# Kernel optimization log

Hardware: AMD Instinct MI355X
Metric: run time of the kernel (lower is better)

Reference implementation:

```python
import jax, jax.numpy as jnp
import numpy as np
import math

EPS = 1.1920929e-07  # torch.finfo(float32).eps, used by nn.RMSNorm when eps=None
N_HEADS = 16

def _rmsnorm(x, w):
    return x * jax.lax.rsqrt(jnp.mean(x * x, axis=-1, keepdims=True) + EPS) * w

def setup_inputs() -> dict:
    key = jax.random.key(0)
    D, V, FF = 1024, 32000, 2048
    NS, IPS = 4, 8
    B, T = 2, 1024
    ks = jax.random.split(key, 8)
    sd = 0.02
    g = lambda i, shape: jax.random.normal(ks[i], shape, jnp.float32) * sd
    return {
        "tokens": jax.random.randint(ks[0], (B, T), 0, V),
        "embed_w": g(1, (V, D)),
        "qkv_w": g(2, (3 * D, D)),
        "o_w": g(3, (D, D)),
        "gate_w": g(4, (FF, D)),
        "up_w": g(5, (FF, D)),
        "down_w": g(6, (D, FF)),
        "norm1_w": jnp.ones((D,), jnp.float32),
        "norm2_w": jnp.ones((D,), jnp.float32),
        "scale_gamma": jnp.ones((NS, D), jnp.float32),
        "scale_beta": jnp.zeros((NS, D), jnp.float32),
        "iter_scale": jnp.ones((NS, IPS), jnp.float32),
        "norm_w": jnp.ones((D,), jnp.float32),
        "lm_head_w": g(7, (V, D)),
    }

def _block(x, gamma, beta, qkv_w, o_w, gate_w, up_w, down_w, norm1_w, norm2_w):
    B, T, D = x.shape
    hd = D // N_HEADS
    # pre-attn norm + FiLM modulation
    h = _rmsnorm(x, norm1_w) * gamma + beta
    qkv = (h @ qkv_w.T).reshape(B, T, 3, N_HEADS, hd)
    q = jnp.transpose(qkv[:, :, 0], (0, 2, 1, 3))  # [B,H,T,hd]
    k = jnp.transpose(qkv[:, :, 1], (0, 2, 1, 3))
    v = jnp.transpose(qkv[:, :, 2], (0, 2, 1, 3))
    scores = jnp.einsum('bhqd,bhkd->bhqk', q, k) / math.sqrt(hd)
    causal = jnp.tril(jnp.ones((T, T), dtype=bool))
    scores = jnp.where(causal, scores, -jnp.inf)
    attn = jax.nn.softmax(scores, axis=-1)
    out = jnp.einsum('bhqk,bhkd->bhqd', attn, v)
    out = jnp.transpose(out, (0, 2, 1, 3)).reshape(B, T, D)
    x = x + out @ o_w.T
    # pre-FFN norm + FiLM modulation, SwiGLU
    h2 = _rmsnorm(x, norm2_w) * gamma + beta
    x = x + (jax.nn.silu(h2 @ gate_w.T) * (h2 @ up_w.T)) @ down_w.T
    return x

def reference(tokens, embed_w, qkv_w, o_w, gate_w, up_w, down_w, norm1_w,
              norm2_w, scale_gamma, scale_beta, iter_scale, norm_w, lm_head_w):
    NS, IPS = iter_scale.shape
    x = embed_w[tokens].astype(jnp.float32)  # [B,T,D]
    # flatten (scale, iter) schedule to per-virtual-layer params [NS*IPS, ...]
    gammas = jnp.repeat(scale_gamma, IPS, axis=0)
    betas = jnp.repeat(scale_beta, IPS, axis=0)
    iters = iter_scale.reshape(-1)

    @jax.checkpoint
    def step(x, per):
        g, b, s = per
        y = _block(x, g, b, qkv_w, o_w, gate_w, up_w, down_w, norm1_w, norm2_w)
        return x + (y - x) * s, None

    x, _ = jax.lax.scan(step, x, (gammas, betas, iters))
    return _rmsnorm(x, norm_w) @ lm_head_w.T  # [B,T,V]
```

## Files before the change

kernel.cpp:

```cpp
#include <hip/hip_runtime.h>

typedef __bf16 bf16;
typedef __attribute__((ext_vector_type(8))) __bf16 bf16x8;
typedef __attribute__((ext_vector_type(4))) __bf16 bf16x4;
typedef __attribute__((ext_vector_type(4))) float f32x4;

#define MFMA16(a,b,c) __builtin_amdgcn_mfma_f32_16x16x32_bf16((a),(b),(c),0,0,0)

__device__ __forceinline__ void gload16(const void* g, void* l) {
    __builtin_amdgcn_global_load_lds((const __attribute__((address_space(1))) void*)g,
                                     (__attribute__((address_space(3))) void*)l, 16, 0, 0);
}

__device__ __forceinline__ int xcd_swizzle(int orig, int nwg) {
    int q = nwg >> 3, r = nwg & 7;
    int xcd = orig & 7, loc = orig >> 3;
    int base = (xcd < r) ? xcd * (q + 1) : r * (q + 1) + (xcd - r) * q;
    return base + loc;
}


__global__ __launch_bounds__(256) void cvt_kernel(const float* __restrict__ in,
                                                  bf16* __restrict__ out, int n4) {
    int stride = gridDim.x * 256;
    for (int i = blockIdx.x * 256 + threadIdx.x; i < n4; i += stride) {
        float4 v = ((const float4*)in)[i];
        bf16x4 o;
        o[0] = (bf16)v.x; o[1] = (bf16)v.y; o[2] = (bf16)v.z; o[3] = (bf16)v.w;
        ((bf16x4*)out)[i] = o;
    }
}

__global__ __launch_bounds__(256) void embed_kernel(const int* __restrict__ tok,
                                                    const float* __restrict__ ew,
                                                    float* __restrict__ X) {
    int m = blockIdx.x;
    int t = tok[m];
    ((float4*)(X + (size_t)m * 1024))[threadIdx.x] =
        ((const float4*)(ew + (size_t)t * 1024))[threadIdx.x];
}

template <bool FILM>
__global__ __launch_bounds__(256) void rmsnorm_kernel(const float* __restrict__ X,
                                                      const float* __restrict__ w,
                                                      const float* __restrict__ gamma,
                                                      const float* __restrict__ beta,
                                                      bf16* __restrict__ H) {
    int m = blockIdx.x, t = threadIdx.x;
    float4 xv = ((const float4*)(X + (size_t)m * 1024))[t];
    float ss = xv.x * xv.x + xv.y * xv.y + xv.z * xv.z + xv.w * xv.w;
#pragma unroll
    for (int off = 1; off < 64; off <<= 1) ss += __shfl_xor(ss, off);
    __shared__ float red[4];
    if ((t & 63) == 0) red[t >> 6] = ss;
    __syncthreads();
    float tot = red[0] + red[1] + red[2] + red[3];
    float sc = rsqrtf(tot * (1.0f / 1024.0f) + 1.1920929e-07f);
    float4 wv = ((const float4*)w)[t];
    float r0 = xv.x * sc * wv.x, r1 = xv.y * sc * wv.y;
    float r2 = xv.z * sc * wv.z, r3 = xv.w * sc * wv.w;
    if (FILM) {
        float4 gv = ((const float4*)gamma)[t];
        float4 bv = ((const float4*)beta)[t];
        r0 = r0 * gv.x + bv.x; r1 = r1 * gv.y + bv.y;
        r2 = r2 * gv.z + bv.z; r3 = r3 * gv.w + bv.w;
    }
    bf16x4 o;
    o[0] = (bf16)r0; o[1] = (bf16)r1; o[2] = (bf16)r2; o[3] = (bf16)r3;
    ((bf16x4*)(H + (size_t)m * 1024))[t] = o;
}


__global__ __launch_bounds__(256) void vtrans_kernel(const bf16* __restrict__ QKV,
                                                     bf16* __restrict__ VT) {
    const int tt = blockIdx.x, bh = blockIdx.y;
    const int b = bh >> 4, h = bh & 15;
    __shared__ __align__(16) bf16 Ls[64 * 72];
    const int tid = threadIdx.x;
#pragma unroll
    for (int i = 0; i < 2; ++i) {
        int cid = tid + 256 * i;
        int r = cid >> 3, c8 = (cid & 7) * 8;
        *(bf16x8*)(Ls + r * 72 + c8) =
            *(const bf16x8*)(QKV + (size_t)(b * 1024 + tt * 64 + r) * 3072 + 2048 + h * 64 + c8);
    }
    __syncthreads();
#pragma unroll
    for (int i = 0; i < 2; ++i) {
        int cid = tid + 256 * i;
        int d = cid >> 3, k8 = (cid & 7) * 8;
        bf16x8 v;
#pragma unroll
        for (int j = 0; j < 8; ++j) v[j] = Ls[(k8 + j) * 72 + d];
        *(bf16x8*)(VT + (size_t)bh * 65536 + (size_t)d * 1024 + tt * 64 + k8) = v;
    }
}


template <int MT, int MODE, bool BNF>
__global__ __launch_bounds__(256, 2) void gemm_bt(const bf16* __restrict__ A,
                                                  const bf16* __restrict__ B,
                                                  int GN, int GM,
                                                  int N, int K,
                                                  bf16* __restrict__ Cb, float* __restrict__ Cf,
                                                  const float* __restrict__ Xin,
                                                  const float* __restrict__ Xin2,
                                                  float* __restrict__ Xout,
                                                  const float* __restrict__ sptr) {
    constexpr int BM = 32 * MT;
    __shared__ __align__(16) bf16 As[2][BM * 64];
    __shared__ __align__(16) bf16 Bs[2][128 * 64];
    const int wg = xcd_swizzle(blockIdx.x, GN * GM);
    int bn, bm;
    if (BNF) { bm = wg / GN; bn = wg - bm * GN; }
    else     { bn = wg / GM; bm = wg - bn * GM; }
    const int tid = threadIdx.x, lane = tid & 63, w = tid >> 6;
    const int wr = w >> 1, wc = w & 1, lr = lane & 15, lg = lane >> 4;
    const bf16* Ab = A + (size_t)bm * BM * K;
    const bf16* Bb = B + (size_t)bn * 128 * K;

    f32x4 acc[MT][4];
#pragma unroll
    for (int i = 0; i < MT; ++i)
#pragma unroll
        for (int j = 0; j < 4; ++j) acc[i][j] = (f32x4){0.f, 0.f, 0.f, 0.f};

#define STAGE_AB(buf, ktv)                                                        \
    do {                                                                          \
        _Pragma("unroll")                                                         \
        for (int i = 0; i < MT; ++i) {                                            \
            int cw = i * 256 + w * 64; int cid = cw + lane;                       \
            gload16(Ab + (size_t)(cid >> 3) * K + (ktv) + (cid & 7) * 8,          \
                    As[buf] + cw * 8);                                            \
        }                                                                         \
        _Pragma("unroll")                                                         \
        for (int i = 0; i < 4; ++i) {                                             \
            int cw = i * 256 + w * 64; int cid = cw + lane;                       \
            gload16(Bb + (size_t)(cid >> 3) * K + (ktv) + (cid & 7) * 8,          \
                    Bs[buf] + cw * 8);                                            \
        }                                                                         \
    } while (0)

    STAGE_AB(0, 0);
    __syncthreads();
    int cur = 0;
    for (int kt = 0; kt < K; kt += 64) {
        if (kt + 64 < K) STAGE_AB(cur ^ 1, kt + 64);
        const bf16* Asc = As[cur];
        const bf16* Bsc = Bs[cur];
#pragma unroll
        for (int kk = 0; kk < 64; kk += 32) {
            bf16x8 af[MT], bfr[4];
#pragma unroll
            for (int mi = 0; mi < MT; ++mi)
                af[mi] = *(const bf16x8*)(Asc + (wr * (16 * MT) + mi * 16 + lr) * 64 + kk + lg * 8);
#pragma unroll
            for (int ni = 0; ni < 4; ++ni)
                bfr[ni] = *(const bf16x8*)(Bsc + (wc * 64 + ni * 16 + lr) * 64 + kk + lg * 8);
#pragma unroll
            for (int mi = 0; mi < MT; ++mi)
#pragma unroll
                for (int ni = 0; ni < 4; ++ni)
                    acc[mi][ni] = MFMA16(af[mi], bfr[ni], acc[mi][ni]);
        }
        __syncthreads();
        cur ^= 1;
    }
#undef STAGE_AB

    float s1 = (MODE == 2) ? sptr[0] : 0.f;
#pragma unroll
    for (int mi = 0; mi < MT; ++mi) {
#pragma unroll
        for (int ni = 0; ni < 4; ++ni) {
#pragma unroll
            for (int j = 0; j < 4; ++j) {
                int row = bm * BM + wr * (16 * MT) + mi * 16 + lg * 4 + j;
                int col = bn * 128 + wc * 64 + ni * 16 + lr;
                size_t idx = (size_t)row * N + col;
                float v = acc[mi][ni][j];
                if (MODE == 0) Cb[idx] = (bf16)v;
                else if (MODE == 1) Xout[idx] = Xin[idx] + v;
                else if (MODE == 2) Xout[idx] = Xin[idx] + s1 * (Xin2[idx] - Xin[idx] + v);
                else Cf[idx] = v;
            }
        }
    }
}


__global__ __launch_bounds__(256, 2) void gemm_gateup(const bf16* __restrict__ A,
                                                      const bf16* __restrict__ Bg,
                                                      const bf16* __restrict__ Bu,
                                                      bf16* __restrict__ FF) {
    const int K = 1024, N = 2048;
    __shared__ __align__(16) bf16 As[2][64 * 64];
    __shared__ __align__(16) bf16 Gs[2][128 * 64];
    __shared__ __align__(16) bf16 Us[2][128 * 64];
    const int wg = xcd_swizzle(blockIdx.x, 512);
    const int bn = wg >> 5, bm = wg & 31;
    const int tid = threadIdx.x, lane = tid & 63, w = tid >> 6;
    const int wr = w >> 1, wc = w & 1, lr = lane & 15, lg = lane >> 4;
    const bf16* Ab = A + (size_t)bm * 64 * K;
    const bf16* Gb = Bg + (size_t)bn * 128 * K;
    const bf16* Ub = Bu + (size_t)bn * 128 * K;

    f32x4 ag[2][4], au[2][4];
#pragma unroll
    for (int i = 0; i < 2; ++i)
#pragma unroll
        for (int j = 0; j < 4; ++j) {
            ag[i][j] = (f32x4){0.f, 0.f, 0.f, 0.f};
            au[i][j] = (f32x4){0.f, 0.f, 0.f, 0.f};
        }

#define STAGE_GU(buf, ktv)                                                        \
    do {                                                                          \
        _Pragma("unroll")                                                         \
        for (int i = 0; i < 2; ++i) {                                             \
            int cw = i * 256 + w * 64; int cid = cw + lane;                       \
            gload16(Ab + (size_t)(cid >> 3) * K + (ktv) + (cid & 7) * 8,          \
                    As[buf] + cw * 8);                                            \
        }                                                                         \
        _Pragma("unroll")                                                         \
        for (int i = 0; i < 4; ++i) {                                             \
            int cw = i * 256 + w * 64; int cid = cw + lane;                       \
            size_t ro = (size_t)(cid >> 3) * K + (ktv) + (cid & 7) * 8;           \
            gload16(Gb + ro, Gs[buf] + cw * 8);                                   \
            gload16(Ub + ro, Us[buf] + cw * 8);                                   \
        }                                                                         \
    } while (0)

    STAGE_GU(0, 0);
    __syncthreads();
    int cur = 0;
    for (int kt = 0; kt < K; kt += 64) {
        if (kt + 64 < K) STAGE_GU(cur ^ 1, kt + 64);
        const bf16* Asc = As[cur];
        const bf16* Gsc = Gs[cur];
        const bf16* Usc = Us[cur];
#pragma unroll
        for (int kk = 0; kk < 64; kk += 32) {
            bf16x8 af[2], gf[4], uf[4];
#pragma unroll
            for (int mi = 0; mi < 2; ++mi)
                af[mi] = *(const bf16x8*)(Asc + (wr * 32 + mi * 16 + lr) * 64 + kk + lg * 8);
#pragma unroll
            for (int ni = 0; ni < 4; ++ni) {
                gf[ni] = *(const bf16x8*)(Gsc + (wc * 64 + ni * 16 + lr) * 64 + kk + lg * 8);
                uf[ni] = *(const bf16x8*)(Usc + (wc * 64 + ni * 16 + lr) * 64 + kk + lg * 8);
            }
#pragma unroll
            for (int mi = 0; mi < 2; ++mi)
#pragma unroll
                for (int ni = 0; ni < 4; ++ni) {
                    ag[mi][ni] = MFMA16(af[mi], gf[ni], ag[mi][ni]);
                    au[mi][ni] = MFMA16(af[mi], uf[ni], au[mi][ni]);
                }
        }
        __syncthreads();
        cur ^= 1;
    }
#undef STAGE_GU

#pragma unroll
    for (int mi = 0; mi < 2; ++mi) {
#pragma unroll
        for (int ni = 0; ni < 4; ++ni) {
#pragma unroll
            for (int j = 0; j < 4; ++j) {
                int row = bm * 64 + wr * 32 + mi * 16 + lg * 4 + j;
                int col = bn * 128 + wc * 64 + ni * 16 + lr;
                float g = ag[mi][ni][j], u = au[mi][ni][j];
                float sg = g / (1.0f + __expf(-g));
                FF[(size_t)row * N + col] = (bf16)(sg * u);
            }
        }
    }
}


__global__ __launch_bounds__(256) void attn_kernel(const bf16* __restrict__ QKV,
                                                   const bf16* __restrict__ VTg,
                                                   bf16* __restrict__ AO) {
    const int qt = blockIdx.x, bh = blockIdx.y;
    const int b = bh >> 4, h = bh & 15;
    const int tid = threadIdx.x;
    const int w = tid >> 6, lane = tid & 63;
    const int lr = lane & 15, lg = lane >> 4;

    __shared__ __align__(16) bf16 Ks[64 * 72];
    __shared__ __align__(16) bf16 Vt[64 * 72];
    __shared__ __align__(16) bf16 Ps[4 * 16 * 72];
    bf16* Pw = Ps + w * 16 * 72;

    const int qrow = b * 1024 + qt * 64 + w * 16 + lr;
    const bf16* qptr = QKV + (size_t)qrow * 3072 + h * 64;
    const bf16* vt_src = VTg + (size_t)bh * 65536;
    bf16x8 qf0 = *(const bf16x8*)(qptr + lg * 8);
    bf16x8 qf1 = *(const bf16x8*)(qptr + 32 + lg * 8);

    f32x4 o[4];
#pragma unroll
    for (int i = 0; i < 4; ++i) o[i] = (f32x4){0.f, 0.f, 0.f, 0.f};
    float m_run = -1e30f, l_run = 0.f;
    const int gq = qt * 64 + w * 16 + lr;

    for (int kt = 0; kt <= qt; ++kt) {
        __syncthreads();
#pragma unroll
        for (int i = 0; i < 2; ++i) {
            int cid = tid + 256 * i;
            int r = cid >> 3, c8 = (cid & 7) * 8;
            const bf16* kvrow = QKV + (size_t)(b * 1024 + kt * 64 + r) * 3072 + h * 64;
            *(bf16x8*)(Ks + r * 72 + c8) = *(const bf16x8*)(kvrow + 1024 + c8);
            *(bf16x8*)(Vt + r * 72 + c8) =
                *(const bf16x8*)(vt_src + (size_t)r * 1024 + kt * 64 + c8);
        }
        __syncthreads();

        f32x4 st[4];
#pragma unroll
        for (int i = 0; i < 4; ++i) st[i] = (f32x4){0.f, 0.f, 0.f, 0.f};
        __builtin_amdgcn_s_setprio(1);
#pragma unroll
        for (int ki = 0; ki < 4; ++ki) {
            bf16x8 kf0 = *(const bf16x8*)(Ks + (ki * 16 + lr) * 72 + lg * 8);
            bf16x8 kf1 = *(const bf16x8*)(Ks + (ki * 16 + lr) * 72 + 32 + lg * 8);
            st[ki] = MFMA16(kf0, qf0, st[ki]);
            st[ki] = MFMA16(kf1, qf1, st[ki]);
        }
        __builtin_amdgcn_s_setprio(0);
        bool diag = (kt == qt);
        float pm = -1e30f;
#pragma unroll
        for (int ki = 0; ki < 4; ++ki) {
#pragma unroll
            for (int j = 0; j < 4; ++j) {
                float sv = st[ki][j] * 0.125f;
                if (diag) {
                    int gk = kt * 64 + ki * 16 + lg * 4 + j;
                    if (gk > gq) sv = -1e30f;
                }
                st[ki][j] = sv;
                pm = fmaxf(pm, sv);
            }
        }
        pm = fmaxf(pm, __shfl_xor(pm, 16));
        pm = fmaxf(pm, __shfl_xor(pm, 32));
        float m_new = fmaxf(m_run, pm);
        float alpha = __expf(m_run - m_new);
        float rs = 0.f;
#pragma unroll
        for (int ki = 0; ki < 4; ++ki) {
            bf16x4 pb;
#pragma unroll
            for (int j = 0; j < 4; ++j) {
                float pv = __expf(st[ki][j] - m_new);
                rs += pv;
                pb[j] = (bf16)pv;
            }
            *(bf16x4*)(Pw + lr * 72 + ki * 16 + lg * 4) = pb;
        }
        rs += __shfl_xor(rs, 16);
        rs += __shfl_xor(rs, 32);
        l_run = l_run * alpha + rs;
        m_run = m_new;
#pragma unroll
        for (int di = 0; di < 4; ++di) o[di] *= alpha;
        __builtin_amdgcn_s_setprio(1);
#pragma unroll
        for (int dk = 0; dk < 2; ++dk) {
            bf16x8 pf = *(const bf16x8*)(Pw + lr * 72 + dk * 32 + lg * 8);
#pragma unroll
            for (int di = 0; di < 4; ++di) {
                bf16x8 vf = *(const bf16x8*)(Vt + (di * 16 + lr) * 72 + dk * 32 + lg * 8);
                o[di] = MFMA16(vf, pf, o[di]);
            }
        }
        __builtin_amdgcn_s_setprio(0);
    }
    float inv = 1.0f / l_run;
    bf16* optr = AO + (size_t)qrow * 1024 + h * 64;
#pragma unroll
    for (int di = 0; di < 4; ++di) {
        bf16x4 ov;
#pragma unroll
        for (int j = 0; j < 4; ++j) ov[j] = (bf16)(o[di][j] * inv);
        *(bf16x4*)(optr + di * 16 + lg * 4) = ov;
    }
}


extern "C" void kernel_launch(void* const* d_in, const int* in_sizes, int n_in,
                              void* d_out, int out_size, void* d_ws, size_t ws_size,
                              hipStream_t stream) {
    const int* tokens = (const int*)d_in[0];
    const float* embed_w = (const float*)d_in[1];
    const float* qkv_w = (const float*)d_in[2];
    const float* o_w = (const float*)d_in[3];
    const float* gate_w = (const float*)d_in[4];
    const float* up_w = (const float*)d_in[5];
    const float* down_w = (const float*)d_in[6];
    const float* norm1_w = (const float*)d_in[7];
    const float* norm2_w = (const float*)d_in[8];
    const float* scale_gamma = (const float*)d_in[9];
    const float* scale_beta = (const float*)d_in[10];
    const float* iter_scale = (const float*)d_in[11];
    const float* norm_w = (const float*)d_in[12];
    const float* lm_head_w = (const float*)d_in[13];

    char* p = (char*)d_ws;
    auto alloc = [&](size_t nbytes) -> char* {
        char* r = p;
        p += (nbytes + 255) & ~(size_t)255;
        return r;
    };
    bf16* WQKV = (bf16*)alloc(3072ull * 1024 * 2);
    bf16* WO   = (bf16*)alloc(1024ull * 1024 * 2);
    bf16* WG   = (bf16*)alloc(2048ull * 1024 * 2);
    bf16* WU   = (bf16*)alloc(2048ull * 1024 * 2);
    bf16* WD   = (bf16*)alloc(1024ull * 2048 * 2);
    bf16* WLM  = (bf16*)alloc(32000ull * 1024 * 2);
    float* X   = (float*)alloc(2048ull * 1024 * 4);
    float* X1  = (float*)alloc(2048ull * 1024 * 4);
    bf16* H    = (bf16*)alloc(2048ull * 1024 * 2);
    bf16* QKVb = (bf16*)alloc(2048ull * 3072 * 2);
    bf16* VT   = (bf16*)alloc(2048ull * 1024 * 2);
    bf16* AO   = (bf16*)alloc(2048ull * 1024 * 2);
    bf16* FF   = (bf16*)alloc(2048ull * 2048 * 2);

    cvt_kernel<<<1024, 256, 0, stream>>>(qkv_w, WQKV, 3072 * 1024 / 4);
    cvt_kernel<<<1024, 256, 0, stream>>>(o_w, WO, 1024 * 1024 / 4);
    cvt_kernel<<<1024, 256, 0, stream>>>(gate_w, WG, 2048 * 1024 / 4);
    cvt_kernel<<<1024, 256, 0, stream>>>(up_w, WU, 2048 * 1024 / 4);
    cvt_kernel<<<1024, 256, 0, stream>>>(down_w, WD, 1024 * 2048 / 4);
    cvt_kernel<<<2048, 256, 0, stream>>>(lm_head_w, WLM, 32000 * 1024 / 4);
    embed_kernel<<<2048, 256, 0, stream>>>(tokens, embed_w, X);

    for (int l = 0; l < 32; ++l) {
        const float* gm = scale_gamma + (size_t)(l >> 3) * 1024;
        const float* bt = scale_beta + (size_t)(l >> 3) * 1024;
        rmsnorm_kernel<true><<<2048, 256, 0, stream>>>(X, norm1_w, gm, bt, H);
        gemm_bt<4, 0, false><<<24 * 16, 256, 0, stream>>>(H, WQKV, 24, 16, 3072, 1024,
                                                          QKVb, nullptr, nullptr, nullptr, nullptr, nullptr);
        vtrans_kernel<<<dim3(16, 32), 256, 0, stream>>>(QKVb, VT);
        attn_kernel<<<dim3(16, 32), 256, 0, stream>>>(QKVb, VT, AO);
        gemm_bt<2, 1, true><<<8 * 32, 256, 0, stream>>>(AO, WO, 8, 32, 1024, 1024,
                                                        nullptr, nullptr, X, nullptr, X1, nullptr);
        rmsnorm_kernel<true><<<2048, 256, 0, stream>>>(X1, norm2_w, gm, bt, H);
        gemm_gateup<<<512, 256, 0, stream>>>(H, WG, WU, FF);
        gemm_bt<2, 2, true><<<8 * 32, 256, 0, stream>>>(FF, WD, 8, 32, 1024, 2048,
                                                        nullptr, nullptr, X, X1, X, iter_scale + l);
    }
    rmsnorm_kernel<false><<<2048, 256, 0, stream>>>(X, norm_w, nullptr, nullptr, H);
    gemm_bt<4, 3, false><<<250 * 16, 256, 0, stream>>>(H, WLM, 250, 16, 32000, 1024,
                                                       nullptr, (float*)d_out, nullptr, nullptr, nullptr, nullptr);
}
```

Before: 5.083 ms.

## Triple-buffer GEMM with vmcnt waits and fix tile height at 64

Reworks gemm_bt to a three-stage LDS ring with loads issued two tiles ahead. It waits on fine-grained s_waitcnt vmcnt counts plus a single raw barrier per k-step instead of a full __syncthreads after each tile. The MT template is removed so every GEMM uses 64-row tiles, doubling the grid for the QKV and LM-head GEMMs. gemm_gateup now issues the next stage before waiting, using explicit vmcnt and barriers. Smaller tiles raise parallelism but reduce reuse of the B operand, and the extra buffer increases LDS use, which may limit occupancy.

```diff
diff --git a/kernel.cpp b/kernel.cpp
--- a/kernel.cpp
+++ b/kernel.cpp
@@ -97,7 +97,7 @@
 }
 
 
-template <int MT, int MODE, bool BNF>
+template <int MODE, bool BNF>
 __global__ __launch_bounds__(256, 2) void gemm_bt(const bf16* __restrict__ A,
                                                   const bf16* __restrict__ B,
                                                   int GN, int GM,
@@ -107,9 +107,9 @@
                                                   const float* __restrict__ Xin2,
                                                   float* __restrict__ Xout,
                                                   const float* __restrict__ sptr) {
-    constexpr int BM = 32 * MT;
-    __shared__ __align__(16) bf16 As[2][BM * 64];
-    __shared__ __align__(16) bf16 Bs[2][128 * 64];
+    constexpr int BM = 64;
+    __shared__ __align__(16) bf16 As[3][BM * 64];
+    __shared__ __align__(16) bf16 Bs[3][128 * 64];
     const int wg = xcd_swizzle(blockIdx.x, GN * GM);
     int bn, bm;
     if (BNF) { bm = wg / GN; bn = wg - bm * GN; }
@@ -119,63 +119,69 @@
     const bf16* Ab = A + (size_t)bm * BM * K;
     const bf16* Bb = B + (size_t)bn * 128 * K;
 
-    f32x4 acc[MT][4];
-#pragma unroll
-    for (int i = 0; i < MT; ++i)
+    f32x4 acc[2][4];
+#pragma unroll
+    for (int i = 0; i < 2; ++i)
 #pragma unroll
         for (int j = 0; j < 4; ++j) acc[i][j] = (f32x4){0.f, 0.f, 0.f, 0.f};
 
 #define STAGE_AB(buf, ktv)                                                        \
     do {                                                                          \
+        bf16* Ad = &As[0][0] + (buf) * (BM * 64);                                 \
+        bf16* Bd = &Bs[0][0] + (buf) * (128 * 64);                                \
         _Pragma("unroll")                                                         \
-        for (int i = 0; i < MT; ++i) {                                            \
+        for (int i = 0; i < 2; ++i) {                                             \
             int cw = i * 256 + w * 64; int cid = cw + lane;                       \
             gload16(Ab + (size_t)(cid >> 3) * K + (ktv) + (cid & 7) * 8,          \
-                    As[buf] + cw * 8);                                            \
+                    Ad + cw * 8);                                                 \
         }                                                                         \
         _Pragma("unroll")                                                         \
         for (int i = 0; i < 4; ++i) {                                             \
             int cw = i * 256 + w * 64; int cid = cw + lane;                       \
             gload16(Bb + (size_t)(cid >> 3) * K + (ktv) + (cid & 7) * 8,          \
-                    Bs[buf] + cw * 8);                                            \
+                    Bd + cw * 8);                                                 \
         }                                                                         \
     } while (0)
 
+    const int nt = K >> 6;
     STAGE_AB(0, 0);
-    __syncthreads();
-    int cur = 0;
-    for (int kt = 0; kt < K; kt += 64) {
-        if (kt + 64 < K) STAGE_AB(cur ^ 1, kt + 64);
-        const bf16* Asc = As[cur];
-        const bf16* Bsc = Bs[cur];
+    STAGE_AB(1, 64);
+    int cur = 0, stg = 2;
+    for (int t = 0; t < nt; ++t) {
+        if (t < nt - 1) asm volatile("s_waitcnt vmcnt(6)" ::: "memory");
+        else            asm volatile("s_waitcnt vmcnt(0)" ::: "memory");
+        __builtin_amdgcn_s_barrier();
+        if (t + 2 < nt) STAGE_AB(stg, (t + 2) * 64);
+        const bf16* Asc = &As[0][0] + cur * (BM * 64);
+        const bf16* Bsc = &Bs[0][0] + cur * (128 * 64);
 #pragma unroll
         for (int kk = 0; kk < 64; kk += 32) {
-            bf16x8 af[MT], bfr[4];
-#pragma unroll
-            for (int mi = 0; mi < MT; ++mi)
-                af[mi] = *(const bf16x8*)(Asc + (wr * (16 * MT) + mi * 16 + lr) * 64 + kk + lg * 8);
+            bf16x8 af[2], bfr[4];
+#pragma unroll
+            for (int mi = 0; mi < 2; ++mi)
+                af[mi] = *(const bf16x8*)(Asc + (wr * 32 + mi * 16 + lr) * 64 + kk + lg * 8);
 #pragma unroll
             for (int ni = 0; ni < 4; ++ni)
                 bfr[ni] = *(const bf16x8*)(Bsc + (wc * 64 + ni * 16 + lr) * 64 + kk + lg * 8);
 #pragma unroll
-            for (int mi = 0; mi < MT; ++mi)
+            for (int mi = 0; mi < 2; ++mi)
 #pragma unroll
                 for (int ni = 0; ni < 4; ++ni)
                     acc[mi][ni] = MFMA16(af[mi], bfr[ni], acc[mi][ni]);
         }
-        __syncthreads();
-        cur ^= 1;
+        cur = (cur == 2) ? 0 : cur + 1;
+        stg = (stg == 2) ? 0 : stg + 1;
     }
 #undef STAGE_AB
 
     float s1 = (MODE == 2) ? sptr[0] : 0.f;
 #pragma unroll
-    for (int mi = 0; mi < MT; ++mi) {
+    for (int mi = 0; mi < 2; ++mi) {
 #pragma unroll
         for (int ni = 0; ni < 4; ++ni) {
 #pragma unroll
             for (int j = 0; j < 4; ++j) {
-                int row = bm * BM + wr * (16 * MT) + mi * 16 + lg * 4 + j;
+                int row = bm * BM + wr * 32 + mi * 16 + lg * 4 + j;
                 int col = bn * 128 + wc * 64 + ni * 16 + lr;
                 size_t idx = (size_t)row * N + col;
                 float v = acc[mi][ni][j];
@@ -232,10 +238,12 @@
     } while (0)
 
     STAGE_GU(0, 0);
-    __syncthreads();
     int cur = 0;
-    for (int kt = 0; kt < K; kt += 64) {
-        if (kt + 64 < K) STAGE_GU(cur ^ 1, kt + 64);
+    for (int t = 0; t < 16; ++t) {
+        if (t + 1 < 16) STAGE_GU(cur ^ 1, (t + 1) * 64);
+        if (t < 15) asm volatile("s_waitcnt vmcnt(10)" ::: "memory");
+        else        asm volatile("s_waitcnt vmcnt(0)" ::: "memory");
+        __builtin_amdgcn_s_barrier();
         const bf16* Asc = As[cur];
         const bf16* Gsc = Gs[cur];
         const bf16* Usc = Us[cur];
@@ -258,7 +266,7 @@
                     au[mi][ni] = MFMA16(af[mi], uf[ni], au[mi][ni]);
                 }
         }
-        __syncthreads();
+        __builtin_amdgcn_s_barrier();
         cur ^= 1;
     }
 #undef STAGE_GU
@@ -442,18 +450,18 @@
         const float* gm = scale_gamma + (size_t)(l >> 3) * 1024;
         const float* bt = scale_beta + (size_t)(l >> 3) * 1024;
         rmsnorm_kernel<true><<<2048, 256, 0, stream>>>(X, norm1_w, gm, bt, H);
-        gemm_bt<4, 0, false><<<24 * 16, 256, 0, stream>>>(H, WQKV, 24, 16, 3072, 1024,
-                                                          QKVb, nullptr, nullptr, nullptr, nullptr, nullptr);
+        gemm_bt<0, false><<<24 * 32, 256, 0, stream>>>(H, WQKV, 24, 32, 3072, 1024,
+                                                       QKVb, nullptr, nullptr, nullptr, nullptr, nullptr);
         vtrans_kernel<<<dim3(16, 32), 256, 0, stream>>>(QKVb, VT);
         attn_kernel<<<dim3(16, 32), 256, 0, stream>>>(QKVb, VT, AO);
-        gemm_bt<2, 1, true><<<8 * 32, 256, 0, stream>>>(AO, WO, 8, 32, 1024, 1024,
-                                                        nullptr, nullptr, X, nullptr, X1, nullptr);
+        gemm_bt<1, true><<<8 * 32, 256, 0, stream>>>(AO, WO, 8, 32, 1024, 1024,
+                                                     nullptr, nullptr, X, nullptr, X1, nullptr);
         rmsnorm_kernel<true><<<2048, 256, 0, stream>>>(X1, norm2_w, gm, bt, H);
         gemm_gateup<<<512, 256, 0, stream>>>(H, WG, WU, FF);
-        gemm_bt<2, 2, true><<<8 * 32, 256, 0, stream>>>(FF, WD, 8, 32, 1024, 2048,
-                                                        nullptr, nullptr, X, X1, X, iter_scale + l);
+        gemm_bt<2, true><<<8 * 32, 256, 0, stream>>>(FF, WD, 8, 32, 1024, 2048,
+                                                     nullptr, nullptr, X, X1, X, iter_scale + l);
     }
     rmsnorm_kernel<false><<<2048, 256, 0, stream>>>(X, norm_w, nullptr, nullptr, H);
-    gemm_bt<4, 3, false><<<250 * 16, 256, 0, stream>>>(H, WLM, 250, 16, 32000, 1024,
-                                                       nullptr, (float*)d_out, nullptr, nullptr, nullptr, nullptr);
-}
+    gemm_bt<3, false><<<250 * 32, 256, 0, stream>>>(H, WLM, 250, 32, 32000, 1024,
+                                                    nullptr, (float*)d_out, nullptr, nullptr, nullptr, nullptr);
+}
```

After: 5.465 ms. 7.5% more time.
